# Kernel optimization log

Measured on AMD Instinct MI355X. Metric: run time of the kernel, lower is better.

The kernel has to match this reference:

```python
import jax, jax.numpy as jnp
import numpy as np

B, S, H = 2, 2048, 1024
NH = 16
HD = H // NH
SCALE = 1.0 / np.sqrt(HD).astype(np.float32)


def setup_inputs() -> dict:
    key = jax.random.key(0)
    ks = jax.random.split(key, 7)
    lim = 1.0 / np.sqrt(H)  # lecun-ish init scale for linear weights
    return {
        "query": jax.random.normal(ks[0], (B, S, H), dtype=jnp.float32),
        "key_in": jax.random.normal(ks[1], (B, S, H), dtype=jnp.float32),
        "value": jax.random.normal(ks[2], (B, S, H), dtype=jnp.float32),
        "attention_mask": jnp.ones((B, S), dtype=jnp.int32),
        "Wq": jax.random.uniform(ks[3], (H, H), jnp.float32, -lim, lim),
        "Wk": jax.random.uniform(ks[4], (H, H), jnp.float32, -lim, lim),
        "Wv": jax.random.uniform(ks[5], (H, H), jnp.float32, -lim, lim),
        "Wo": jax.random.uniform(ks[6], (H, H), jnp.float32, -lim, lim),
    }


def reference(query, key_in, value, attention_mask, Wq, Wk, Wv, Wo):
    b, s, _ = query.shape
    # projections (no bias)
    q = (query @ Wq).reshape(b, s, NH, HD).transpose(0, 2, 1, 3)  # [b,h,s,d]
    k = (key_in @ Wk).reshape(b, s, NH, HD).transpose(0, 2, 1, 3)
    v = (value @ Wv).reshape(b, s, NH, HD).transpose(0, 2, 1, 3)

    scores = jnp.einsum("bhqd,bhkd->bhqk", q, k) * SCALE  # [b,h,s,s]
    mask = attention_mask[:, None, None, :]  # broadcast over heads & query pos
    scores = jnp.where(mask == 0, -1e9, scores)
    attn = jax.nn.softmax(scores, axis=-1)

    ctx = jnp.einsum("bhqk,bhkd->bhqd", attn, v)
    ctx = ctx.transpose(0, 2, 1, 3).reshape(b, s, H)
    out = ctx @ Wo
    return out, jnp.mean(attn, axis=1)
```

## Files before the change

kernel.cpp:

```cpp
#include <hip/hip_runtime.h>
#include <stdint.h>

#define BB 2
#define SS 2048
#define HH 1024
#define NHEAD 16
#define HDIM 64

constexpr int   BSROWS = BB * SS;
constexpr float SCALE  = 0.125f;
constexpr float LOG2E  = 1.4426950408889634f;
constexpr float SL     = SCALE * LOG2E;

typedef __bf16 bf16;
typedef __attribute__((ext_vector_type(8))) __bf16 bf16x8;
typedef __attribute__((ext_vector_type(4))) __bf16 bf16x4;
typedef __attribute__((ext_vector_type(4))) float  f32x4;

#define MFMA16(a, b, c) __builtin_amdgcn_mfma_f32_16x16x32_bf16((a), (b), (c), 0, 0, 0)

__device__ __forceinline__ void gload_lds16(const void* g, void* l) {
  __builtin_amdgcn_global_load_lds((const __attribute__((address_space(1))) void*)g,
                                   (__attribute__((address_space(3))) void*)l, 16, 0, 0);
}

__global__ __launch_bounds__(256) void cvt_in(const float* __restrict__ q, const float* __restrict__ k,
                                              const float* __restrict__ v, const int* __restrict__ mask,
                                              bf16* __restrict__ xq, bf16* __restrict__ xk,
                                              bf16* __restrict__ xv, float* __restrict__ bias2) {
  int i = blockIdx.x * 256 + threadIdx.x;
  int e = i * 4;
  f32x4 a = *(const f32x4*)(q + e);
  f32x4 b = *(const f32x4*)(k + e);
  f32x4 c = *(const f32x4*)(v + e);
  *(bf16x4*)(xq + e) = __builtin_convertvector(a, bf16x4);
  *(bf16x4*)(xk + e) = __builtin_convertvector(b, bf16x4);
  *(bf16x4*)(xv + e) = __builtin_convertvector(c, bf16x4);
  if (i < BB * SS) bias2[i] = mask[i] ? 0.0f : -1e9f * LOG2E;
}

__global__ __launch_bounds__(256) void cvt_wt(const float* __restrict__ Wq, const float* __restrict__ Wk,
                                              const float* __restrict__ Wv, const float* __restrict__ Wo,
                                              bf16* __restrict__ Wt) {
  __shared__ float tile[32][33];
  int z = blockIdx.z;
  const float* W = (z == 0) ? Wq : (z == 1) ? Wk : (z == 2) ? Wv : Wo;
  bf16* out = Wt + (size_t)z * HH * HH;
  int bx = blockIdx.x * 32, by = blockIdx.y * 32;
  int tx = threadIdx.x, ty = threadIdx.y;
#pragma unroll
  for (int j = 0; j < 32; j += 8)
    tile[ty + j][tx] = W[(size_t)(by + ty + j) * HH + bx + tx];
  __syncthreads();
#pragma unroll
  for (int j = 0; j < 32; j += 8)
    out[(size_t)(bx + ty + j) * HH + by + tx] = (bf16)tile[tx][ty + j];
}

__global__ __launch_bounds__(256) void gemm128(const bf16* __restrict__ Abase, const bf16* __restrict__ Btbase,
                                               bf16* __restrict__ Qo, bf16* __restrict__ Ko,
                                               bf16* __restrict__ Vto, float* __restrict__ outF, int mode) {
  int zmode = (mode < 0) ? (int)blockIdx.z : mode;
  const bf16* A  = Abase  + (mode < 0 ? (size_t)blockIdx.z * BSROWS * HH : 0);
  const bf16* Bt = Btbase + (mode < 0 ? (size_t)blockIdx.z * HH * HH : 0);

  __shared__ __align__(16) bf16 lA[128 * 32];
  __shared__ __align__(16) bf16 lB[128 * 32];

  int t = threadIdx.x;
  int w = t >> 6, l = t & 63, lg = l >> 4, lr = l & 15;
  int m0 = blockIdx.y * 128, n0 = blockIdx.x * 128;
  int wr = (w >> 1) * 64, wc = (w & 1) * 64;

  f32x4 zero4 = {0.f, 0.f, 0.f, 0.f};
  f32x4 acc[4][4];
#pragma unroll
  for (int i = 0; i < 4; i++)
#pragma unroll
    for (int j = 0; j < 4; j++) acc[i][j] = zero4;

  for (int k0 = 0; k0 < HH; k0 += 32) {
#pragma unroll
    for (int i = 0; i < 2; i++) {
      int idx = i * 256 + t;
      gload_lds16(A  + (size_t)(m0 + (idx >> 2)) * HH + k0 + (idx & 3) * 8, &lA[(i * 256 + w * 64) * 8]);
      gload_lds16(Bt + (size_t)(n0 + (idx >> 2)) * HH + k0 + (idx & 3) * 8, &lB[(i * 256 + w * 64) * 8]);
    }
    __syncthreads();
    bf16x8 af[4], bq[4];
#pragma unroll
    for (int mi = 0; mi < 4; mi++) af[mi] = *(const bf16x8*)&lA[(wr + mi * 16 + lr) * 32 + lg * 8];
#pragma unroll
    for (int ni = 0; ni < 4; ni++) bq[ni] = *(const bf16x8*)&lB[(wc + ni * 16 + lr) * 32 + lg * 8];
#pragma unroll
    for (int mi = 0; mi < 4; mi++)
#pragma unroll
      for (int ni = 0; ni < 4; ni++)
        acc[mi][ni] = MFMA16(af[mi], bq[ni], acc[mi][ni]);
    __syncthreads();
  }

#pragma unroll
  for (int mi = 0; mi < 4; mi++) {
    int row0 = m0 + wr + mi * 16 + lg * 4;
#pragma unroll
    for (int ni = 0; ni < 4; ni++) {
      int col = n0 + wc + ni * 16 + lr;
      if (zmode == 3) {
#pragma unroll
        for (int r = 0; r < 4; r++) outF[(size_t)(row0 + r) * HH + col] = acc[mi][ni][r];
      } else if (zmode == 2) {
        int b = row0 >> 11, s0 = row0 & (SS - 1);
        int h = col >> 6, d = col & 63;
        bf16x4 pk;
#pragma unroll
        for (int r = 0; r < 4; r++) pk[r] = (bf16)acc[mi][ni][r];
        *(bf16x4*)&Vto[((size_t)(b * NHEAD + h) * HDIM + d) * SS + s0] = pk;
      } else {
        bf16* dst = (zmode == 0) ? Qo : Ko;
        int h = col >> 6, d = col & 63;
#pragma unroll
        for (int r = 0; r < 4; r++) {
          int row = row0 + r;
          int b = row >> 11, s = row & (SS - 1);
          dst[((size_t)(b * NHEAD + h) * SS + s) * HDIM + d] = (bf16)acc[mi][ni][r];
        }
      }
    }
  }
}

__global__ __launch_bounds__(256, 2) void attn_pv(const bf16* __restrict__ Q, const bf16* __restrict__ K,
                                                  const bf16* __restrict__ Vt, const float* __restrict__ bias2,
                                                  float* __restrict__ invl, bf16* __restrict__ ctx) {
  int b = blockIdx.z, h = blockIdx.y, q0 = blockIdx.x * 128;
  int t = threadIdx.x, w = t >> 6, l = t & 63, lg = l >> 4, lr = l & 15;
  size_t hb = ((size_t)b * NHEAD + h) * SS;
  const bf16* Qh = Q + hb * HDIM;
  const bf16* Kh = K + hb * HDIM;
  const bf16* Vh = Vt + ((size_t)b * NHEAD + h) * HDIM * SS;
  const float* biasb = bias2 + b * SS;

  __shared__ __align__(16) bf16 sK[64][72];
  __shared__ __align__(16) bf16 sV[64][72];
  __shared__ __align__(16) bf16 lp[4][32][72];

  int r0 = t >> 3, c0 = (t & 7) * 8;
  bf16x8 kreg[2], vreg[2];

  int qa = q0 + w * 32;
  int rowa = qa + lr, rowb = qa + 16 + lr;
  bf16x8 qf0a = *(const bf16x8*)&Qh[(size_t)rowa * HDIM + lg * 8];
  bf16x8 qf1a = *(const bf16x8*)&Qh[(size_t)rowa * HDIM + 32 + lg * 8];
  bf16x8 qf0b = *(const bf16x8*)&Qh[(size_t)rowb * HDIM + lg * 8];
  bf16x8 qf1b = *(const bf16x8*)&Qh[(size_t)rowb * HDIM + 32 + lg * 8];

  f32x4 zero4 = {0.f, 0.f, 0.f, 0.f};
  f32x4 lacca = zero4, laccb = zero4;
  f32x4 ctxa[4], ctxb[4];
#pragma unroll
  for (int nd = 0; nd < 4; nd++) { ctxa[nd] = zero4; ctxb[nd] = zero4; }

#pragma unroll
  for (int i = 0; i < 2; i++) {
    int row = i * 32 + r0;
    kreg[i] = *(const bf16x8*)&Kh[(size_t)row * HDIM + c0];
    vreg[i] = *(const bf16x8*)&Vh[(size_t)row * SS + c0];
  }
#pragma unroll
  for (int i = 0; i < 2; i++) {
    int row = i * 32 + r0;
    *(bf16x8*)&sK[row][c0] = kreg[i];
    *(bf16x8*)&sV[row][c0] = vreg[i];
  }

  for (int kt = 0; kt < 32; kt++) {
    int k0 = kt * 64;
    __syncthreads();
    if (kt < 31) {
      int kn = k0 + 64;
#pragma unroll
      for (int i = 0; i < 2; i++) {
        int row = i * 32 + r0;
        kreg[i] = *(const bf16x8*)&Kh[(size_t)(kn + row) * HDIM + c0];
        vreg[i] = *(const bf16x8*)&Vh[(size_t)row * SS + kn + c0];
      }
    }
    f32x4 acca[4], accb[4];
#pragma unroll
    for (int ni = 0; ni < 4; ni++) {
      const bf16* kp = &sK[ni * 16 + lr][lg * 8];
      bf16x8 kf0 = *(const bf16x8*)kp;
      bf16x8 kf1 = *(const bf16x8*)(kp + 32);
      acca[ni] = MFMA16(kf1, qf1a, MFMA16(kf0, qf0a, zero4));
      accb[ni] = MFMA16(kf1, qf1b, MFMA16(kf0, qf0b, zero4));
    }
    f32x4 pa4[4], pb4[4];
#pragma unroll
    for (int ni = 0; ni < 4; ni++) {
      f32x4 bv = *(const f32x4*)&biasb[k0 + ni * 16 + lg * 4];
      f32x4 za = acca[ni] * SL + bv;
      f32x4 zb = accb[ni] * SL + bv;
#pragma unroll
      for (int r = 0; r < 4; r++) {
        pa4[ni][r] = __builtin_amdgcn_exp2f(za[r]);
        pb4[ni][r] = __builtin_amdgcn_exp2f(zb[r]);
      }
    }
    lacca += (pa4[0] + pa4[1]) + (pa4[2] + pa4[3]);
    laccb += (pb4[0] + pb4[1]) + (pb4[2] + pb4[3]);
#pragma unroll
    for (int ni = 0; ni < 4; ni++) {
      *(bf16x4*)&lp[w][lr][ni * 16 + lg * 4]      = __builtin_convertvector(pa4[ni], bf16x4);
      *(bf16x4*)&lp[w][16 + lr][ni * 16 + lg * 4] = __builtin_convertvector(pb4[ni], bf16x4);
    }
#pragma unroll
    for (int kk = 0; kk < 2; kk++) {
      bf16x8 paa = *(const bf16x8*)&lp[w][lr][kk * 32 + lg * 8];
      bf16x8 pab = *(const bf16x8*)&lp[w][16 + lr][kk * 32 + lg * 8];
#pragma unroll
      for (int nd = 0; nd < 4; nd++) {
        bf16x8 vf = *(const bf16x8*)&sV[nd * 16 + lr][kk * 32 + lg * 8];
        ctxa[nd] = MFMA16(paa, vf, ctxa[nd]);
        ctxb[nd] = MFMA16(pab, vf, ctxb[nd]);
      }
    }
    __syncthreads();
    if (kt < 31) {
#pragma unroll
      for (int i = 0; i < 2; i++) {
        int row = i * 32 + r0;
        *(bf16x8*)&sK[row][c0] = kreg[i];
        *(bf16x8*)&sV[row][c0] = vreg[i];
      }
    }
  }

  float lsa = (lacca[0] + lacca[1]) + (lacca[2] + lacca[3]);
  float lsb = (laccb[0] + laccb[1]) + (laccb[2] + laccb[3]);
  lsa += __shfl_xor(lsa, 16); lsa += __shfl_xor(lsa, 32);
  lsb += __shfl_xor(lsb, 16); lsb += __shfl_xor(lsb, 32);
  float ila = 1.0f / lsa, ilb = 1.0f / lsb;
  f32x4 ilva, ilvb;
#pragma unroll
  for (int r = 0; r < 4; r++) { ilva[r] = __shfl(ila, lg * 4 + r); ilvb[r] = __shfl(ilb, lg * 4 + r); }
#pragma unroll
  for (int nd = 0; nd < 4; nd++)
#pragma unroll
    for (int r = 0; r < 4; r++) {
      int ra = qa + lg * 4 + r, rb = qa + 16 + lg * 4 + r;
      ctx[(size_t)(b * SS + ra) * HH + h * HDIM + nd * 16 + lr] = (bf16)(ctxa[nd][r] * ilva[r]);
      ctx[(size_t)(b * SS + rb) * HH + h * HDIM + nd * 16 + lr] = (bf16)(ctxb[nd][r] * ilvb[r]);
    }
  if (l < 16) {
    invl[hb + qa + l]      = ila;
    invl[hb + qa + 16 + l] = ilb;
  }
}

__global__ __launch_bounds__(256, 4) void attn_mean(const bf16* __restrict__ Q, const bf16* __restrict__ K,
                                                    const float* __restrict__ bias2,
                                                    const float* __restrict__ invl, float* __restrict__ meanOut) {
  int q0 = blockIdx.x * 128, kc0 = blockIdx.y * 64, b = blockIdx.z;
  int t = threadIdx.x, w = t >> 6, l = t & 63, lg = l >> 4, lr = l & 15;
  const float* biasb = bias2 + b * SS;
  __shared__ __align__(16) bf16 sK[4][64][72];
  bf16 (*sKw)[72] = sK[w];

  int qa = q0 + w * 32;
  int rowa = qa + lr, rowb = qa + 16 + lr;
  int sr = (l >> 3), sc = (l & 7) * 8;

  f32x4 zero4 = {0.f, 0.f, 0.f, 0.f};
  f32x4 macca[4], maccb[4];
#pragma unroll
  for (int ni = 0; ni < 4; ni++) { macca[ni] = zero4; maccb[ni] = zero4; }

  bf16x8 kreg[8];
  {
    const bf16* Kh0 = K + ((size_t)b * NHEAD) * SS * HDIM;
#pragma unroll
    for (int j = 0; j < 8; j++)
      kreg[j] = *(const bf16x8*)&Kh0[(size_t)(kc0 + sr + 8 * j) * HDIM + sc];
#pragma unroll
    for (int j = 0; j < 8; j++)
      *(bf16x8*)&sKw[sr + 8 * j][sc] = kreg[j];
  }

  for (int h = 0; h < NHEAD; h++) {
    size_t hb = ((size_t)b * NHEAD + h) * SS;
    const bf16* Qh = Q + hb * HDIM;
    bf16x8 qf0a = *(const bf16x8*)&Qh[(size_t)rowa * HDIM + lg * 8];
    bf16x8 qf1a = *(const bf16x8*)&Qh[(size_t)rowa * HDIM + 32 + lg * 8];
    bf16x8 qf0b = *(const bf16x8*)&Qh[(size_t)rowb * HDIM + lg * 8];
    bf16x8 qf1b = *(const bf16x8*)&Qh[(size_t)rowb * HDIM + 32 + lg * 8];
    float ila = invl[hb + rowa] * (1.0f / NHEAD);
    float ilb = invl[hb + rowb] * (1.0f / NHEAD);
    if (h < NHEAD - 1) {
      const bf16* Khn = K + ((size_t)b * NHEAD + h + 1) * SS * HDIM;
#pragma unroll
      for (int j = 0; j < 8; j++)
        kreg[j] = *(const bf16x8*)&Khn[(size_t)(kc0 + sr + 8 * j) * HDIM + sc];
    }
#pragma unroll
    for (int ni = 0; ni < 4; ni++) {
      const bf16* kp = &sKw[ni * 16 + lr][lg * 8];
      bf16x8 kf0 = *(const bf16x8*)kp;
      bf16x8 kf1 = *(const bf16x8*)(kp + 32);
      f32x4 acca = MFMA16(kf1, qf1a, MFMA16(kf0, qf0a, zero4));
      f32x4 accb = MFMA16(kf1, qf1b, MFMA16(kf0, qf0b, zero4));
      f32x4 bv = *(const f32x4*)&biasb[kc0 + ni * 16 + lg * 4];
      f32x4 za = acca * SL + bv;
      f32x4 zb = accb * SL + bv;
#pragma unroll
      for (int r = 0; r < 4; r++) {
        macca[ni][r] += __builtin_amdgcn_exp2f(za[r]) * ila;
        maccb[ni][r] += __builtin_amdgcn_exp2f(zb[r]) * ilb;
      }
    }
    if (h < NHEAD - 1) {
#pragma unroll
      for (int j = 0; j < 8; j++)
        *(bf16x8*)&sKw[sr + 8 * j][sc] = kreg[j];
    }
  }
  float* meanB = meanOut + (size_t)b * SS * SS;
#pragma unroll
  for (int ni = 0; ni < 4; ni++) {
    *(f32x4*)&meanB[(size_t)rowa * SS + kc0 + ni * 16 + lg * 4] = macca[ni];
    *(f32x4*)&meanB[(size_t)rowb * SS + kc0 + ni * 16 + lg * 4] = maccb[ni];
  }
}

extern "C" void kernel_launch(void* const* d_in, const int* in_sizes, int n_in,
                              void* d_out, int out_size, void* d_ws, size_t ws_size,
                              hipStream_t stream) {
  const float* query  = (const float*)d_in[0];
  const float* key_in = (const float*)d_in[1];
  const float* value  = (const float*)d_in[2];
  const int*   mask   = (const int*)d_in[3];
  const float* Wq     = (const float*)d_in[4];
  const float* Wk     = (const float*)d_in[5];
  const float* Wv     = (const float*)d_in[6];
  const float* Wo     = (const float*)d_in[7];

  char* ws = (char*)d_ws;
  bf16*  Xb    = (bf16*)(ws);
  bf16*  Wt    = (bf16*)(ws + 25165824);
  bf16*  Qb    = (bf16*)(ws + 33554432);
  bf16*  Kb    = (bf16*)(ws + 41943040);
  bf16*  Vtb   = (bf16*)(ws + 50331648);
  float* invlb = (float*)(ws + 58982400);
  float* biasb = (float*)(ws + 59244544);
  bf16*  ctxb  = Xb;

  float* outF  = (float*)d_out;
  float* meanF = outF + (size_t)BB * SS * HH;

  cvt_in<<<4096, 256, 0, stream>>>(query, key_in, value, mask,
                                   Xb, Xb + 4194304, Xb + 8388608, biasb);
  cvt_wt<<<dim3(32, 32, 4), dim3(32, 8), 0, stream>>>(Wq, Wk, Wv, Wo, Wt);
  gemm128<<<dim3(8, 32, 3), 256, 0, stream>>>(Xb, Wt, Qb, Kb, Vtb, nullptr, -1);
  attn_pv<<<dim3(16, 16, 2), 256, 0, stream>>>(Qb, Kb, Vtb, biasb, invlb, ctxb);
  attn_mean<<<dim3(16, 32, 2), 256, 0, stream>>>(Qb, Kb, biasb, invlb, meanF);
  gemm128<<<dim3(8, 32, 1), 256, 0, stream>>>(ctxb, Wt + 3 * (size_t)HH * HH,
                                              nullptr, nullptr, nullptr, outF, 3);
}
```

Measured before the change: 217.8 us.

## Share K tile across warps with double-buffered LDS in attn_mean

Previously each of the four warps loaded its own private copy of the same 64-row K tile into LDS per head, which quadrupled global loads and LDS footprint. Now the whole block cooperatively loads one shared tile into a two-slot buffer, prefetching the next head into registers while computing the current one. A __syncthreads per head is added. Launch bounds are raised to 6 blocks per CU to exploit the smaller LDS and register footprint.

```diff
diff --git a/kernel.cpp b/kernel.cpp
--- a/kernel.cpp
+++ b/kernel.cpp
@@ -258,37 +258,41 @@
   }
 }
 
-__global__ __launch_bounds__(256, 4) void attn_mean(const bf16* __restrict__ Q, const bf16* __restrict__ K,
+__global__ __launch_bounds__(256, 6) void attn_mean(const bf16* __restrict__ Q, const bf16* __restrict__ K,
                                                     const float* __restrict__ bias2,
                                                     const float* __restrict__ invl, float* __restrict__ meanOut) {
   int q0 = blockIdx.x * 128, kc0 = blockIdx.y * 64, b = blockIdx.z;
   int t = threadIdx.x, w = t >> 6, l = t & 63, lg = l >> 4, lr = l & 15;
   const float* biasb = bias2 + b * SS;
-  __shared__ __align__(16) bf16 sK[4][64][72];
-  bf16 (*sKw)[72] = sK[w];
+  __shared__ __align__(16) bf16 sK[2][64][72];
 
   int qa = q0 + w * 32;
   int rowa = qa + lr, rowb = qa + 16 + lr;
-  int sr = (l >> 3), sc = (l & 7) * 8;
+  int sr = t >> 3, sc = (t & 7) * 8;
 
   f32x4 zero4 = {0.f, 0.f, 0.f, 0.f};
   f32x4 macca[4], maccb[4];
 #pragma unroll
   for (int ni = 0; ni < 4; ni++) { macca[ni] = zero4; maccb[ni] = zero4; }
 
-  bf16x8 kreg[8];
+  bf16x8 kreg0, kreg1;
   {
     const bf16* Kh0 = K + ((size_t)b * NHEAD) * SS * HDIM;
-#pragma unroll
-    for (int j = 0; j < 8; j++)
-      kreg[j] = *(const bf16x8*)&Kh0[(size_t)(kc0 + sr + 8 * j) * HDIM + sc];
-#pragma unroll
-    for (int j = 0; j < 8; j++)
-      *(bf16x8*)&sKw[sr + 8 * j][sc] = kreg[j];
-  }
+    kreg0 = *(const bf16x8*)&Kh0[(size_t)(kc0 + sr) * HDIM + sc];
+    kreg1 = *(const bf16x8*)&Kh0[(size_t)(kc0 + sr + 32) * HDIM + sc];
+    *(bf16x8*)&sK[0][sr][sc]      = kreg0;
+    *(bf16x8*)&sK[0][sr + 32][sc] = kreg1;
+  }
+  __syncthreads();
 
   for (int h = 0; h < NHEAD; h++) {
+    int cur = h & 1;
     size_t hb = ((size_t)b * NHEAD + h) * SS;
+    if (h < NHEAD - 1) {
+      const bf16* Khn = K + ((size_t)b * NHEAD + h + 1) * SS * HDIM;
+      kreg0 = *(const bf16x8*)&Khn[(size_t)(kc0 + sr) * HDIM + sc];
+      kreg1 = *(const bf16x8*)&Khn[(size_t)(kc0 + sr + 32) * HDIM + sc];
+    }
     const bf16* Qh = Q + hb * HDIM;
     bf16x8 qf0a = *(const bf16x8*)&Qh[(size_t)rowa * HDIM + lg * 8];
     bf16x8 qf1a = *(const bf16x8*)&Qh[(size_t)rowa * HDIM + 32 + lg * 8];
@@ -296,15 +300,9 @@
     bf16x8 qf1b = *(const bf16x8*)&Qh[(size_t)rowb * HDIM + 32 + lg * 8];
     float ila = invl[hb + rowa] * (1.0f / NHEAD);
     float ilb = invl[hb + rowb] * (1.0f / NHEAD);
-    if (h < NHEAD - 1) {
-      const bf16* Khn = K + ((size_t)b * NHEAD + h + 1) * SS * HDIM;
-#pragma unroll
-      for (int j = 0; j < 8; j++)
-        kreg[j] = *(const bf16x8*)&Khn[(size_t)(kc0 + sr + 8 * j) * HDIM + sc];
-    }
-#pragma unroll
-    for (int ni = 0; ni < 4; ni++) {
-      const bf16* kp = &sKw[ni * 16 + lr][lg * 8];
+#pragma unroll
+    for (int ni = 0; ni < 4; ni++) {
+      const bf16* kp = &sK[cur][ni * 16 + lr][lg * 8];
       bf16x8 kf0 = *(const bf16x8*)kp;
       bf16x8 kf1 = *(const bf16x8*)(kp + 32);
       f32x4 acca = MFMA16(kf1, qf1a, MFMA16(kf0, qf0a, zero4));
@@ -319,9 +317,9 @@
       }
     }
     if (h < NHEAD - 1) {
-#pragma unroll
-      for (int j = 0; j < 8; j++)
-        *(bf16x8*)&sKw[sr + 8 * j][sc] = kreg[j];
+      *(bf16x8*)&sK[cur ^ 1][sr][sc]      = kreg0;
+      *(bf16x8*)&sK[cur ^ 1][sr + 32][sc] = kreg1;
+      __syncthreads();
     }
   }
   float* meanB = meanOut + (size_t)b * SS * SS;
```

Measured after the change: 258.4 us. 1.19x slower.
